# Performance work log

Hardware: AMD Instinct MI355X
Metric: run time of the kernel (lower is better)

The kernel has to match this reference:

```python
import jax, jax.numpy as jnp
import numpy as np

N_NODES = 100000
N_EDGES = 1600000
N_GRAPHS = 1024


def gcn_conv(x, src, dst, W, b, num_nodes):
    # GCNConv: x' = D^{-1/2} (A + I) D^{-1/2} x W + b  (self-loops already appended to src/dst)
    h = x @ W  # [N, out]
    deg = jax.ops.segment_sum(jnp.ones_like(dst, dtype=h.dtype), dst, num_segments=num_nodes)
    dinv = jnp.where(deg > 0, jax.lax.rsqrt(jnp.maximum(deg, 1.0)), 0.0)
    norm = dinv[src] * dinv[dst]  # [E]
    msg = h[src] * norm[:, None]  # [E, out]  <- dominant memory traffic
    return jax.ops.segment_sum(msg, dst, num_segments=num_nodes) + b


def global_mean_pool(x, batch, num_graphs):
    s = jax.ops.segment_sum(x, batch, num_segments=num_graphs)
    cnt = jax.ops.segment_sum(jnp.ones((x.shape[0],), x.dtype), batch, num_segments=num_graphs)
    return s / jnp.maximum(cnt, 1.0)[:, None]


def setup_inputs() -> dict:
    key = jax.random.key(0)
    ks = jax.random.split(key, 12)
    x = jax.random.normal(ks[0], (N_NODES, 4), dtype=jnp.float32)
    edge_index = jax.random.randint(ks[1], (2, N_EDGES), 0, N_NODES, dtype=jnp.int64)
    batch = jnp.sort(jax.random.randint(ks[2], (N_NODES,), 0, N_GRAPHS, dtype=jnp.int64))
    def glorot(k, shape):
        fan = shape[0] + shape[1]
        return jax.random.normal(k, shape, jnp.float32) * jnp.sqrt(2.0 / fan)
    return {
        "x": x, "edge_index": edge_index, "batch": batch,
        "W1": glorot(ks[3], (4, 64)),   "b1": jnp.zeros((64,), jnp.float32),
        "W2": glorot(ks[4], (64, 128)), "b2": jnp.zeros((128,), jnp.float32),
        "fc1_W": glorot(ks[5], (128, 64)), "fc1_b": jnp.zeros((64,), jnp.float32),
        "fc2_W": glorot(ks[6], (64, 1)),   "fc2_b": jnp.zeros((1,), jnp.float32),
    }


def reference(x, edge_index, batch, W1, b1, W2, b2, fc1_W, fc1_b, fc2_W, fc2_b):
    n = x.shape[0]
    loops = jnp.arange(n, dtype=edge_index.dtype)
    src = jnp.concatenate([edge_index[0], loops])
    dst = jnp.concatenate([edge_index[1], loops])
    h = jax.nn.relu(gcn_conv(x, src, dst, W1, b1, n))
    h = jax.nn.relu(gcn_conv(h, src, dst, W2, b2, n))
    g = global_mean_pool(h, batch, N_GRAPHS)  # [G, 128]
    g = jax.nn.relu(g @ fc1_W + fc1_b)
    return g @ fc2_W + fc2_b  # [G, 1]
```

## Files before the change

kernel.cpp:

```cpp
#include <hip/hip_runtime.h>
#include <math.h>


#define EPB 8192
#define BSH 8
#define NBUK_MAX 512

__global__ void k_bukhist(const int* __restrict__ dst, int E,
                          int* __restrict__ bkcnt, int nbuk) {
  __shared__ int hist[NBUK_MAX];
  for (int i = threadIdx.x; i < nbuk; i += blockDim.x) hist[i] = 0;
  __syncthreads();
  int i0 = blockIdx.x * EPB, i1 = min(i0 + EPB, E);
  for (int i = i0 + threadIdx.x; i < i1; i += blockDim.x)
    atomicAdd(&hist[dst[i] >> BSH], 1);
  __syncthreads();
  for (int i = threadIdx.x; i < nbuk; i += blockDim.x)
    if (hist[i]) atomicAdd(&bkcnt[i], hist[i]);
}

__global__ void k_scan_buk(const int* __restrict__ bkcnt, int* __restrict__ bcur,
                           int nbuk) {
  __shared__ int sh[NBUK_MAX];
  int t = threadIdx.x;
  int v = (t < nbuk) ? bkcnt[t] : 0;
  sh[t] = v;
  __syncthreads();
  for (int o = 1; o < NBUK_MAX; o <<= 1) {
    int u = (t >= o) ? sh[t - o] : 0;
    __syncthreads();
    sh[t] += u;
    __syncthreads();
  }
  if (t < nbuk) bcur[t] = sh[t] - v;
}

__global__ void k_bucket(const int* __restrict__ src, const int* __restrict__ dst,
                         int E, int* __restrict__ bcur, int* __restrict__ ebuf,
                         int nbuk) {
  __shared__ int hist[NBUK_MAX];
  __shared__ int hbase[NBUK_MAX];
  int t = threadIdx.x;
  int i0 = blockIdx.x * EPB, i1 = min(i0 + EPB, E);
  for (int i = t; i < nbuk; i += blockDim.x) hist[i] = 0;
  __syncthreads();
  for (int i = i0 + t; i < i1; i += blockDim.x)
    atomicAdd(&hist[dst[i] >> BSH], 1);
  __syncthreads();
  for (int i = t; i < nbuk; i += blockDim.x) {
    int c = hist[i];
    hbase[i] = c ? atomicAdd(&bcur[i], c) : 0;
  }
  __syncthreads();
  for (int i = t; i < nbuk; i += blockDim.x) hist[i] = 0;
  __syncthreads();
  for (int i = i0 + t; i < i1; i += blockDim.x) {
    int d = dst[i];
    int b = d >> BSH;
    int pos = hbase[b] + atomicAdd(&hist[b], 1);
    ebuf[pos] = src[i] | ((d & 255) << 17);
  }
}

__global__ void __launch_bounds__(256) k_sortfill(
    const int* __restrict__ ebuf, const int* __restrict__ bcur,
    const float* __restrict__ x, int* __restrict__ row_ptr,
    int* __restrict__ csr_src, float* __restrict__ dinv,
    float* __restrict__ xp, int N, int nbuk) {
  __shared__ int hist[256];
  __shared__ int sc[256];
  __shared__ int cur[256];
  int b = blockIdx.x, t = threadIdx.x;
  int e0 = (b == 0) ? 0 : bcur[b - 1];
  int e1 = bcur[b];
  hist[t] = 0;
  __syncthreads();
  for (int i = e0 + t; i < e1; i += 256)
    atomicAdd(&hist[ebuf[i] >> 17], 1);
  __syncthreads();
  int v = hist[t];
  sc[t] = v;
  __syncthreads();
  for (int o = 1; o < 256; o <<= 1) {
    int u = (t >= o) ? sc[t - o] : 0;
    __syncthreads();
    sc[t] += u;
    __syncthreads();
  }
  int excl = sc[t] - v;
  int node = (b << BSH) + t;
  if (node < N) {
    row_ptr[node] = e0 + excl;
    float di = 1.0f / sqrtf((float)(v + 1));
    dinv[node] = di;
    float4 xv = ((const float4*)x)[node];
    xv.x *= di; xv.y *= di; xv.z *= di; xv.w *= di;
    ((float4*)xp)[node] = xv;
  }
  if (b == nbuk - 1 && t == 0) row_ptr[N] = e1;
  cur[t] = excl;
  __syncthreads();
  for (int i = e0 + t; i < e1; i += 256) {
    int e = ebuf[i];
    int pos = e0 + atomicAdd(&cur[e >> 17], 1);
    csr_src[pos] = e & 0x1FFFF;
  }
}

__global__ void k_conv1(const float* __restrict__ xp, const int* __restrict__ row_ptr,
                        const int* __restrict__ csr_src, const float* __restrict__ dinv,
                        const float* __restrict__ W1, const float* __restrict__ b1,
                        float* __restrict__ h1ps, int N) {
  int lane = threadIdx.x & 63;
  int sub = lane >> 4, sl = lane & 15;
  int wid = (blockIdx.x * blockDim.x + threadIdx.x) >> 6;
  int nw = (gridDim.x * blockDim.x) >> 6;
  const float4* x4 = (const float4*)xp;
  float w1 = W1[lane], w2 = W1[64 + lane], w3 = W1[128 + lane], w4 = W1[192 + lane];
  float bb = b1[lane];
  size_t slice_off = (size_t)(lane >> 3) * N * 8 + (lane & 7);
  for (int base = wid * 4; base < N; base += nw * 4) {
    int n = base + sub;
    bool valid = (n < N);
    int e0 = 0, e1 = 0;
    if (valid) { e0 = row_ptr[n]; e1 = row_ptr[n + 1]; }
    float ax = 0.f, ay = 0.f, az = 0.f, aw = 0.f;
    for (int j = e0 + sl; j < e1; j += 16) {
      float4 xs = x4[csr_src[j]];
      ax += xs.x; ay += xs.y; az += xs.z; aw += xs.w;
    }
#pragma unroll
    for (int o = 8; o; o >>= 1) {
      ax += __shfl_xor(ax, o); ay += __shfl_xor(ay, o);
      az += __shfl_xor(az, o); aw += __shfl_xor(aw, o);
    }
    float di = 0.f;
    if (valid) {
      di = dinv[n];
      float4 xn = x4[n];
      ax += xn.x; ay += xn.y; az += xn.z; aw += xn.w;
    }
#pragma unroll
    for (int g = 0; g < 4; ++g) {
      int nn = base + g;
      if (nn < N) {
        int srcl = g * 16;
        float bx = __shfl(ax, srcl), by = __shfl(ay, srcl);
        float bz = __shfl(az, srcl), bw = __shfl(aw, srcl);
        float dg = __shfl(di, srcl);
        float o0 = bb;
        o0 = fmaf(bx * dg, w1, o0);
        o0 = fmaf(by * dg, w2, o0);
        o0 = fmaf(bz * dg, w3, o0);
        o0 = fmaf(bw * dg, w4, o0);
        h1ps[slice_off + (size_t)nn * 8] = fmaxf(o0, 0.f) * dg;
      }
    }
  }
}

__global__ void __launch_bounds__(256) k_agg2s(
    const float* __restrict__ h1ps, const int* __restrict__ row_ptr,
    const int* __restrict__ csr_src, const float* __restrict__ dinv,
    float* __restrict__ aggs, int N) {
  int s = blockIdx.x & 7;
  int blk = blockIdx.x >> 3;
  int nblk = gridDim.x >> 3;
  const float* __restrict__ hs = h1ps + (size_t)s * N * 8;
  float* __restrict__ as = aggs + (size_t)s * N * 8;
  int lane = threadIdx.x & 63;
  int sub = lane >> 3;
  int c = lane & 7;
  int wv = threadIdx.x >> 6;
  for (int base = blk * 32 + wv * 8; base < N; base += nblk * 32) {
    int n = base + sub;
    if (n < N) {
      int e0 = row_ptr[n], e1 = row_ptr[n + 1];
      float a0 = 0.f, a1 = 0.f, a2 = 0.f, a3 = 0.f;
      int j = e0;
      for (; j + 4 <= e1; j += 4) {
        int s0 = csr_src[j], s1 = csr_src[j + 1];
        int s2 = csr_src[j + 2], s3 = csr_src[j + 3];
        a0 += hs[(size_t)s0 * 8 + c]; a1 += hs[(size_t)s1 * 8 + c];
        a2 += hs[(size_t)s2 * 8 + c]; a3 += hs[(size_t)s3 * 8 + c];
      }
      for (; j < e1; ++j) a0 += hs[(size_t)csr_src[j] * 8 + c];
      float acc = (a0 + a1) + (a2 + a3);
      acc += hs[(size_t)n * 8 + c];
      as[(size_t)n * 8 + c] = acc * dinv[n];
    }
  }
}

__global__ void __launch_bounds__(256, 4) k_mm2pool(
    const float* __restrict__ aggs, const int* __restrict__ batch,
    const float* __restrict__ W2, const float* __restrict__ b2,
    float* __restrict__ gsum, int N) {
  __shared__ float aT[64][36];
  __shared__ int gid_s[32];
  int tid = threadIdx.x;
  int base = blockIdx.x * 32;
  const float4* a4 = (const float4*)aggs;
  for (int idx = tid; idx < 512; idx += 256) {
    int s = idx >> 6;
    int o = idx & 63;
    int node = o >> 1, h4 = o & 1;
    int n = base + node;
    float4 v = make_float4(0.f, 0.f, 0.f, 0.f);
    if (n < N) v = a4[((size_t)s * N + n) * 2 + h4];
    int ch = s * 8 + h4 * 4;
    aT[ch + 0][node] = v.x;
    aT[ch + 1][node] = v.y;
    aT[ch + 2][node] = v.z;
    aT[ch + 3][node] = v.w;
  }
  if (tid < 32) {
    int n = base + tid;
    gid_s[tid] = (n < N) ? batch[n] : -1;
  }
  __syncthreads();
  int c = tid & 127;
  int g = tid >> 7;
  float acc[16];
#pragma unroll
  for (int i = 0; i < 16; ++i) acc[i] = 0.f;
#pragma unroll 4
  for (int k = 0; k < 64; ++k) {
    float w = W2[k * 128 + c];
    const float4* ap = (const float4*)&aT[k][g * 16];
    float4 v0 = ap[0], v1 = ap[1], v2 = ap[2], v3 = ap[3];
    acc[0] = fmaf(v0.x, w, acc[0]);  acc[1] = fmaf(v0.y, w, acc[1]);
    acc[2] = fmaf(v0.z, w, acc[2]);  acc[3] = fmaf(v0.w, w, acc[3]);
    acc[4] = fmaf(v1.x, w, acc[4]);  acc[5] = fmaf(v1.y, w, acc[5]);
    acc[6] = fmaf(v1.z, w, acc[6]);  acc[7] = fmaf(v1.w, w, acc[7]);
    acc[8] = fmaf(v2.x, w, acc[8]);  acc[9] = fmaf(v2.y, w, acc[9]);
    acc[10] = fmaf(v2.z, w, acc[10]); acc[11] = fmaf(v2.w, w, acc[11]);
    acc[12] = fmaf(v3.x, w, acc[12]); acc[13] = fmaf(v3.y, w, acc[13]);
    acc[14] = fmaf(v3.z, w, acc[14]); acc[15] = fmaf(v3.w, w, acc[15]);
  }
  float bias = b2[c];
  float run = 0.f;
  int cur = -1;
#pragma unroll
  for (int i = 0; i < 16; ++i) {
    int n = base + g * 16 + i;
    if (n < N) {
      int gg = gid_s[g * 16 + i];
      float v = fmaxf(acc[i] + bias, 0.f);
      if (gg == cur) {
        run += v;
      } else {
        if (cur >= 0) atomicAdd(&gsum[(size_t)cur * 128 + c], run);
        cur = gg;
        run = v;
      }
    }
  }
  if (cur >= 0) atomicAdd(&gsum[(size_t)cur * 128 + c], run);
}

__device__ __forceinline__ int lower_bound(const int* __restrict__ a, int n, int key) {
  int lo = 0, hi = n;
  while (lo < hi) {
    int m = (lo + hi) >> 1;
    if (a[m] < key) lo = m + 1; else hi = m;
  }
  return lo;
}

__global__ void k_fc(const float* __restrict__ gsum, const int* __restrict__ batch,
                     const float* __restrict__ fc1W, const float* __restrict__ fc1b,
                     const float* __restrict__ fc2W, const float* __restrict__ fc2b,
                     float* __restrict__ out, int N, int G) {
  int g = blockIdx.x;
  int tid = threadIdx.x;
  __shared__ int bnd[2];
  if (tid == 0) bnd[0] = lower_bound(batch, N, g);
  if (tid == 1) bnd[1] = lower_bound(batch, N, g + 1);
  __shared__ float grow[128];
  __syncthreads();
  int cnt = bnd[1] - bnd[0];
  float inv = 1.0f / (float)max(cnt, 1);
  grow[tid] = gsum[(size_t)g * 128 + tid] * inv;
  __syncthreads();
  if (tid < 64) {
    float o = fc1b[tid];
#pragma unroll 8
    for (int k = 0; k < 128; ++k) o = fmaf(grow[k], fc1W[k * 64 + tid], o);
    o = fmaxf(o, 0.f);
    float v = o * fc2W[tid];
#pragma unroll
    for (int off = 32; off; off >>= 1) v += __shfl_xor(v, off);
    if (tid == 0) out[g] = v + fc2b[0];
  }
}

extern "C" void kernel_launch(void* const* d_in, const int* in_sizes, int n_in,
                              void* d_out, int out_size, void* d_ws, size_t ws_size,
                              hipStream_t stream) {
  const float* x = (const float*)d_in[0];
  const int* ei = (const int*)d_in[1];
  const int* batch = (const int*)d_in[2];
  const float* W1 = (const float*)d_in[3];
  const float* b1 = (const float*)d_in[4];
  const float* W2 = (const float*)d_in[5];
  const float* b2 = (const float*)d_in[6];
  const float* fc1W = (const float*)d_in[7];
  const float* fc1b = (const float*)d_in[8];
  const float* fc2W = (const float*)d_in[9];
  const float* fc2b = (const float*)d_in[10];
  float* out = (float*)d_out;

  int N = in_sizes[0] / 4;
  int E = in_sizes[1] / 2;
  int G = out_size;
  const int* src = ei;
  const int* dst = ei + E;

  char* ws = (char*)d_ws;
  size_t off = 0;
  auto take = [&](size_t b) {
    char* p = ws + off;
    off += (b + 255) & ~(size_t)255;
    return p;
  };
  int nbuk = (N + 255) >> BSH;
  int ebl = (E + EPB - 1) / EPB;
  int* row_ptr  = (int*)take((size_t)(N + 1) * 4);
  int* bkcnt    = (int*)take((size_t)NBUK_MAX * 4);
  int* bcur     = (int*)take((size_t)NBUK_MAX * 4);
  float* dinv   = (float*)take((size_t)N * 4);
  float* xp     = (float*)take((size_t)N * 4 * 4);
  int* ebuf     = (int*)take((size_t)E * 4);
  int* csr_src  = (int*)take((size_t)E * 4);
  float* h1ps   = (float*)take((size_t)N * 64 * 4);
  float* aggs   = (float*)take((size_t)N * 64 * 4);
  float* gsum   = (float*)take((size_t)G * 128 * 4);
  (void)ws_size;

  hipMemsetAsync(bkcnt, 0, (size_t)NBUK_MAX * 4, stream);
  hipMemsetAsync(gsum, 0, (size_t)G * 128 * 4, stream);

  k_bukhist<<<ebl, 256, 0, stream>>>(dst, E, bkcnt, nbuk);
  k_scan_buk<<<1, NBUK_MAX, 0, stream>>>(bkcnt, bcur, nbuk);
  k_bucket<<<ebl, 256, 0, stream>>>(src, dst, E, bcur, ebuf, nbuk);
  k_sortfill<<<nbuk, 256, 0, stream>>>(ebuf, bcur, x, row_ptr, csr_src, dinv, xp, N, nbuk);

  k_conv1<<<2048, 256, 0, stream>>>(xp, row_ptr, csr_src, dinv, W1, b1, h1ps, N);
  int aggblk = ((N + 31) / 32) * 8;
  k_agg2s<<<aggblk, 256, 0, stream>>>(h1ps, row_ptr, csr_src, dinv, aggs, N);
  k_mm2pool<<<(N + 31) / 32, 256, 0, stream>>>(aggs, batch, W2, b2, gsum, N);
  k_fc<<<G, 128, 0, stream>>>(gsum, batch, fc1W, fc1b, fc2W, fc2b, out, N, G);
}
```

Before: 290.1 us.

## Assign one wavefront per node in layer-2 aggregation with shuffle reduction

The layer-2 neighbor aggregation changes from 8 nodes per wavefront (8 lanes per node, each walking all of that node's edges serially) to one node per wavefront. The 8 edge groups split the edge list and are combined with xor shuffles. This shortens each lane's serial gather chain and exposes more memory-level parallelism per node. In exchange it launches 8x more blocks, leaves lanes idle when a node has fewer than 8 edges (average degree is about 17), and drops the grid-stride loop.

Result: slower. 395.0 us (+36.2%).

```diff
diff --git a/kernel.cpp b/kernel.cpp
--- a/kernel.cpp
+++ b/kernel.cpp
@@ -164,31 +164,28 @@
     const int* __restrict__ csr_src, const float* __restrict__ dinv,
     float* __restrict__ aggs, int N) {
   int s = blockIdx.x & 7;
-  int blk = blockIdx.x >> 3;
-  int nblk = gridDim.x >> 3;
+  int node = (blockIdx.x >> 3) * 4 + (threadIdx.x >> 6);
+  if (node >= N) return;
   const float* __restrict__ hs = h1ps + (size_t)s * N * 8;
   float* __restrict__ as = aggs + (size_t)s * N * 8;
   int lane = threadIdx.x & 63;
-  int sub = lane >> 3;
-  int c = lane & 7;
-  int wv = threadIdx.x >> 6;
-  for (int base = blk * 32 + wv * 8; base < N; base += nblk * 32) {
-    int n = base + sub;
-    if (n < N) {
-      int e0 = row_ptr[n], e1 = row_ptr[n + 1];
-      float a0 = 0.f, a1 = 0.f, a2 = 0.f, a3 = 0.f;
-      int j = e0;
-      for (; j + 4 <= e1; j += 4) {
-        int s0 = csr_src[j], s1 = csr_src[j + 1];
-        int s2 = csr_src[j + 2], s3 = csr_src[j + 3];
-        a0 += hs[(size_t)s0 * 8 + c]; a1 += hs[(size_t)s1 * 8 + c];
-        a2 += hs[(size_t)s2 * 8 + c]; a3 += hs[(size_t)s3 * 8 + c];
-      }
-      for (; j < e1; ++j) a0 += hs[(size_t)csr_src[j] * 8 + c];
-      float acc = (a0 + a1) + (a2 + a3);
-      acc += hs[(size_t)n * 8 + c];
-      as[(size_t)n * 8 + c] = acc * dinv[n];
-    }
+  int eg = lane >> 3, c = lane & 7;
+  int e0 = row_ptr[node], e1 = row_ptr[node + 1];
+  float a0 = 0.f, a1 = 0.f;
+  int j = e0 + eg;
+  for (; j + 8 < e1; j += 16) {
+    int i0 = csr_src[j], i1 = csr_src[j + 8];
+    a0 += hs[(size_t)i0 * 8 + c];
+    a1 += hs[(size_t)i1 * 8 + c];
+  }
+  if (j < e1) a0 += hs[(size_t)csr_src[j] * 8 + c];
+  float acc = a0 + a1;
+  acc += __shfl_xor(acc, 8);
+  acc += __shfl_xor(acc, 16);
+  acc += __shfl_xor(acc, 32);
+  if (eg == 0) {
+    acc += hs[(size_t)node * 8 + c];
+    as[(size_t)node * 8 + c] = acc * dinv[node];
   }
 }
 
@@ -347,7 +344,7 @@
   k_sortfill<<<nbuk, 256, 0, stream>>>(ebuf, bcur, x, row_ptr, csr_src, dinv, xp, N, nbuk);
 
   k_conv1<<<2048, 256, 0, stream>>>(xp, row_ptr, csr_src, dinv, W1, b1, h1ps, N);
-  int aggblk = ((N + 31) / 32) * 8;
+  int aggblk = ((N + 3) / 4) * 8;
   k_agg2s<<<aggblk, 256, 0, stream>>>(h1ps, row_ptr, csr_src, dinv, aggs, N);
   k_mm2pool<<<(N + 31) / 32, 256, 0, stream>>>(aggs, batch, W2, b2, gsum, N);
   k_fc<<<G, 128, 0, stream>>>(gsum, batch, fc1W, fc1b, fc2W, fc2b, out, N, G);
```
